# Kernel tuning notes

Hardware: AMD Instinct MI355X
Metric: run time of the kernel (lower is better)

The kernel has to match this reference:

```python
import jax, jax.numpy as jnp
from jax import lax
import numpy as np

B, CIN, H, S = 32, 16, 64, 128
TAU = 0.5


def _conv1d(x, w, b, dilation):
    # x: [B, C, S], w: [O, I, K] -> [B, O, S], stride 1, SAME padding (matches torch padding='same')
    y = lax.conv_general_dilated(x, w, window_strides=(1,), padding='SAME',
                                 rhs_dilation=(dilation,),
                                 dimension_numbers=('NCH', 'OIH', 'NCH'))
    return y + b[None, :, None]


def setup_inputs() -> dict:
    key = jax.random.key(0)
    ks = jax.random.split(key, 16)
    def w(k, shape, fan_in):
        return jax.random.normal(k, shape, jnp.float32) * (1.0 / np.sqrt(fan_in))
    inp = {
        'data': jax.random.normal(ks[0], (B, 1, CIN, S), jnp.float32),
        'conv11_w': w(ks[1], (H, CIN, 1), CIN), 'conv11_b': jnp.zeros((H,), jnp.float32),
        'conv12_w': w(ks[2], (H, H, 3), H * 3), 'conv12_b': jnp.zeros((H,), jnp.float32),
        'conv21_w': w(ks[3], (H, CIN, 1), CIN), 'conv21_b': jnp.zeros((H,), jnp.float32),
        'conv22_w': w(ks[4], (H, H, 5), H * 5), 'conv22_b': jnp.zeros((H,), jnp.float32),
        'conv31_w': w(ks[5], (H, CIN, 5), CIN * 5), 'conv31_b': jnp.zeros((H,), jnp.float32),
        'fc_final_w': w(ks[6], (H, 3 * H), 3 * H), 'fc_final_b': jnp.zeros((H,), jnp.float32),
        'fc1_w': w(ks[7], (H, 2 * H), 2 * H), 'fc1_b': jnp.zeros((H,), jnp.float32),
        'fc2_w': w(ks[8], (2, H), H), 'fc2_b': jnp.zeros((2,), jnp.float32),
        # pre-sampled uniform noise for gumbel-softmax (deterministic reference)
        'gumbel_u': jax.random.uniform(ks[9], (B, S * S, 2), jnp.float32, 1e-7, 1.0 - 1e-7),
    }
    return inp


def reference(data, conv11_w, conv11_b, conv12_w, conv12_b, conv21_w, conv21_b,
              conv22_w, conv22_b, conv31_w, conv31_b, fc_final_w, fc_final_b,
              fc1_w, fc1_b, fc2_w, fc2_b, gumbel_u):
    x = data[:, 0].astype(jnp.float32)                      # [B, CIN, S]
    x1 = _conv1d(_conv1d(x, conv11_w, conv11_b, 1), conv12_w, conv12_b, 3)
    x2 = _conv1d(_conv1d(x, conv21_w, conv21_b, 1), conv22_w, conv22_b, 5)
    x3 = _conv1d(x, conv31_w, conv31_b, 1)
    h = jnp.concatenate([x1, x2, x3], axis=1)               # [B, 3H, S]
    h = jnp.swapaxes(h, 1, 2)                               # [B, S, 3H]
    h = jax.nn.relu(h @ fc_final_w.T + fc_final_b)          # [B, S, H]

    # one-hot matmuls are exact gathers: rec rows = repeat, send cols = tile
    rows = jnp.repeat(jnp.arange(S), S)                     # [S*S]
    cols = jnp.tile(jnp.arange(S), S)                       # [S*S]
    receivers = h[:, rows]                                  # [B, S*S, H]
    senders = h[:, cols]                                    # [B, S*S, H]
    e = jnp.concatenate([senders, receivers], axis=2)       # [B, S*S, 2H]
    e = jax.nn.relu(e @ fc1_w.T + fc1_b)
    logits = e @ fc2_w.T + fc2_b                            # [B, S*S, 2]

    # gumbel-softmax, hard=True (straight-through)
    g = -jnp.log(-jnp.log(gumbel_u))
    y_soft = jax.nn.softmax((logits + g) / TAU, axis=-1)
    y_hard = jax.nn.one_hot(jnp.argmax(y_soft, axis=-1), 2, dtype=y_soft.dtype)
    y = lax.stop_gradient(y_hard - y_soft) + y_soft

    a = y[..., 0].reshape(-1, S, S)                         # [B, S, S]
    keep = jnp.triu(jnp.ones((S, S), bool), k=1)            # zero lower tri and diagonal
    return jnp.where(keep, a, jnp.zeros((), a.dtype))
```

## Files before the change

kernel.cpp:

```cpp
#include <hip/hip_runtime.h>
#include <math.h>

#define BB   32
#define CIN  16
#define HH   64
#define SS   128

typedef double f64x4 __attribute__((ext_vector_type(4)));
#define MFMA64(a,b,c) __builtin_amdgcn_mfma_f64_16x16x4f64((a),(b),(c),0,0,0)

__global__ __launch_bounds__(256) void prep_weights(
    const float* __restrict__ w11, const float* __restrict__ w21,
    const float* __restrict__ w12, const float* __restrict__ w22,
    const float* __restrict__ w31, const float* __restrict__ wf,
    const float* __restrict__ w1,  float* __restrict__ W)
{
    int i = blockIdx.x * 256 + threadIdx.x;
    if (i < 1024)       { int k=i>>4, c=i&15;                  W[c*64+k]          = w11[i]; }
    else if (i < 2048)  { int j=i-1024;  int k=j>>4, c=j&15;   W[1024 + c*64+k]   = w21[j]; }
    else if (i < 14336) { int j=i-2048;  int n=j/192, r=j-192*n; W[2048 + r*64+n] = w12[j]; }
    else if (i < 34816) { int j=i-14336; int n=j/320, r=j-320*n; W[14336 + r*64+n]= w22[j]; }
    else if (i < 43008) { int j=i-34816; int r=j>>6, n=j&63;   W[34816 + j] = (r<80)? w31[n*80+r] : 0.f; }
    else if (i < 55296) { int j=i-43008; int n=j/192, r=j-192*n; W[43008 + r*64+n]= wf[j]; }
    else if (i < 59392) { int j=i-55296; int n=j>>6, m=j&63;   W[55296 + m*64+n]  = w1[n*128+m]; }
    else if (i < 63488) { int j=i-59392; int n=j>>6, m=j&63;   W[59392 + m*64+n]  = w1[n*128+64+m]; }
}

__device__ __forceinline__ void issue_pf(float* pf, const float* __restrict__ Wsrc,
                                         int c, int t) {
    if (c < 15) {
        const float* s = Wsrc + 2048 + c * 4096 + t;
        #pragma unroll
        for (int q = 0; q < 16; ++q) pf[q] = s[q * 256];
    }
}
__device__ __forceinline__ void commit_pf(const float* pf, double* Wf, int t,
                                          int mB1, int mB2) {
    #pragma unroll
    for (int q = 0; q < 16; ++q) {
        int e = t + 256 * q, k = e >> 6, n = e & 63;
        Wf[((k>>2)<<8) + ((n>>4)<<6) + (k&3)*mB1 + (n&15)*mB2] = (double)pf[q];
    }
}
__device__ __forceinline__ void mfma_chunk(const double* pA, const double* pB,
                                           f64x4& a0, f64x4& a1, f64x4& a2, f64x4& a3) {
    #pragma unroll
    for (int s = 0; s < 16; s += 4) {
        a0 = MFMA64(pA[(s+0)*64], pB[(s+0)*256], a0);
        a1 = MFMA64(pA[(s+1)*64], pB[(s+1)*256], a1);
        a2 = MFMA64(pA[(s+2)*64], pB[(s+2)*256], a2);
        a3 = MFMA64(pA[(s+3)*64], pB[(s+3)*256], a3);
    }
}

#define RUN_PHASE(NCH, ABASE, ...) do {                                        \
    f64x4 ac0{0,0,0,0}, ac1{0,0,0,0}, ac2{0,0,0,0}, ac3{0,0,0,0};              \
    for (int ch_ = 0; ch_ < (NCH); ++ch_) {                                    \
        commit_pf(pf, Wf, t, mB1, mB2);                                        \
        __syncthreads();                                                       \
        ++cc; issue_pf(pf, Wsrc, cc, t);                                       \
        mfma_chunk((ABASE) + ch_*1024 + lane, Wf + wofs + lane,                \
                   ac0, ac1, ac2, ac3);                                        \
        __syncthreads();                                                       \
    }                                                                          \
    f64x4 acm = (ac0 + ac1) + (ac2 + ac3);                                     \
    __VA_ARGS__                                                                \
} while (0)

__global__ __launch_bounds__(256, 1) void fused_front(
    const float* __restrict__ x,
    const float* __restrict__ b11, const float* __restrict__ b12,
    const float* __restrict__ b21, const float* __restrict__ b22,
    const float* __restrict__ b31, const float* __restrict__ bf,
    const float* __restrict__ b1,  const float* __restrict__ Wsrc,
    double* __restrict__ Qg, double* __restrict__ Pg)
{
    const int b  = blockIdx.y;
    const int s0 = blockIdx.x * 16;
    const int t  = threadIdx.x;
    const int lane = t & 63, wave = t >> 6, wofs = wave << 6;

    __shared__ float  xl[CIN][37];
    __shared__ double t1e[48 * 64];
    __shared__ double t2e[80 * 64];
    __shared__ double x3e[32 * 64];
    __shared__ double Wf[4096];
    __shared__ double x123[16][196];
    double* he = x3e;

    int rowi[4], colj[4], mA1, mA2, mB1, mB2;
    {
        double lv = (double)lane;
        f64x4 zz{0.0, 0.0, 0.0, 0.0};
        f64x4 d1 = MFMA64(lv, 1.0, zz);
        f64x4 d2 = MFMA64(1.0, lv, zz);
        int am = ((((int)d1[0]) & 3) == 0);
        int bm = ((((int)d2[0]) & 3) == 0);
        for (int r = 0; r < 4; ++r) {
            int v1 = (int)d1[r], v2 = (int)d2[r];
            rowi[r] = (am ? (v1 - 96) >> 2 : (v1 - 6) >> 4) & 15;
            colj[r] = (bm ? (v2 - 96) >> 2 : (v2 - 6) >> 4) & 15;
        }
        mA1 = am ? 16 : 1;  mA2 = am ? 1 : 4;
        mB1 = bm ? 16 : 1;  mB2 = bm ? 1 : 4;
    }

    float pf[16];
    int cc = 0;
    issue_pf(pf, Wsrc, 0, t);

    float* wA = (float*)Wf;
    for (int e = t; e < 2048; e += 256) wA[e] = Wsrc[e];
    for (int e = t; e < CIN * 36; e += 256) {
        int c = e / 36, col = e - c * 36;
        int g = s0 - 10 + col;
        xl[c][col] = (g >= 0 && g < SS) ? x[(b * CIN + c) * SS + g] : 0.f;
    }
    __syncthreads();

    for (int e = t; e < 1408; e += 256) {
        int k = e & 63, col = e >> 6;
        int g = s0 - 3 + col;
        double val = 0.0;
        if (g >= 0 && g < SS) {
            double u0 = (double)b11[k], u1 = 0.0;
            #pragma unroll
            for (int c = 0; c < CIN; c += 2) {
                u0 += (double)xl[c][col + 7]     * (double)wA[c * 64 + k];
                u1 += (double)xl[c + 1][col + 7] * (double)wA[(c + 1) * 64 + k];
            }
            val = u0 + u1;
        }
        #pragma unroll
        for (int tp = 0; tp < 3; ++tp) {
            int p = col - 3 * tp;
            if (p >= 0 && p < 16) {
                int kk = k * 3 + tp;
                t1e[((kk>>2)<<6) + (kk&3)*mA1 + p*mA2] = val;
            }
        }
    }
    for (int e = t; e < 2304; e += 256) {
        int k = e & 63, col = e >> 6;
        int g = s0 - 10 + col;
        double val = 0.0;
        if (g >= 0 && g < SS) {
            double u0 = (double)b21[k], u1 = 0.0;
            #pragma unroll
            for (int c = 0; c < CIN; c += 2) {
                u0 += (double)xl[c][col]     * (double)wA[1024 + c * 64 + k];
                u1 += (double)xl[c + 1][col] * (double)wA[1024 + (c + 1) * 64 + k];
            }
            val = u0 + u1;
        }
        #pragma unroll
        for (int tp = 0; tp < 5; ++tp) {
            int p = col - 5 * tp;
            if (p >= 0 && p < 16) {
                int kk = k * 5 + tp;
                t2e[((kk>>2)<<6) + (kk&3)*mA1 + p*mA2] = val;
            }
        }
    }
    for (int e = t; e < 2048; e += 256) {
        int p = e & 15, kk = e >> 4;
        double val = 0.0;
        if (kk < 80) { int c = kk / 5, tp = kk - c * 5; val = (double)xl[c][p + 8 + tp]; }
        x3e[((kk>>2)<<6) + (kk&3)*mA1 + p*mA2] = val;
    }
    __syncthreads();

    RUN_PHASE(3, t1e, {
        for (int r = 0; r < 4; ++r) {
            int ch = (wave << 4) + colj[r];
            x123[rowi[r]][ch] = acm[r] + (double)b12[ch];
        }
    });
    RUN_PHASE(5, t2e, {
        for (int r = 0; r < 4; ++r) {
            int ch = (wave << 4) + colj[r];
            x123[rowi[r]][64 + ch] = acm[r] + (double)b22[ch];
        }
    });
    RUN_PHASE(2, x3e, {
        for (int r = 0; r < 4; ++r) {
            int ch = (wave << 4) + colj[r];
            x123[rowi[r]][128 + ch] = acm[r] + (double)b31[ch];
        }
    });
    __syncthreads();
    for (int e = t; e < 3072; e += 256) {
        int p = e & 15, k = e >> 4;
        t1e[((k>>2)<<6) + (k&3)*mA1 + p*mA2] = x123[p][k];
    }
    __syncthreads();
    RUN_PHASE(3, t1e, {
        for (int r = 0; r < 4; ++r) {
            int m = (wave << 4) + colj[r];
            double v = acm[r] + (double)bf[m];
            he[((m>>2)<<6) + (m&3)*mA1 + rowi[r]*mA2] = v > 0.0 ? v : 0.0;
        }
    });
    RUN_PHASE(1, he, {
        for (int r = 0; r < 4; ++r)
            Qg[((long)b * SS + s0 + rowi[r]) * HH + (wave << 4) + colj[r]] = acm[r];
    });
    RUN_PHASE(1, he, {
        for (int r = 0; r < 4; ++r) {
            int ch = (wave << 4) + colj[r];
            Pg[((long)b * SS + s0 + rowi[r]) * HH + ch] = acm[r] + (double)b1[ch];
        }
    });
}

__global__ __launch_bounds__(256) void edges(
    const double* __restrict__ Qg, const double* __restrict__ Pg,
    const float* __restrict__ w2, const float* __restrict__ b2,
    const float* __restrict__ gum, float* __restrict__ out)
{
    const int b   = blockIdx.y;
    const int tit = blockIdx.x >> 3;
    const int tjt = blockIdx.x & 7;
    const int t   = threadIdx.x;
    const int ti  = t >> 4, tj = t & 15;
    const int i   = tit * 16 + ti;
    const int j   = tjt * 16 + tj;
    float* op = out + ((long)b * SS + i) * SS + j;

    if (tjt < tit) { *op = 0.0f; return; }

    __shared__ double Pl[16][66];
    __shared__ double Ql[16][66];
    __shared__ double dwl[64];

    if (t < 64) dwl[t] = (double)w2[t] - (double)w2[64 + t];
    for (int idx = t; idx < 1024; idx += 256) {
        int r = idx >> 6, c = idx & 63;
        Pl[r][c] = Pg[((long)b * SS + tit * 16 + r) * HH + c];
        Ql[r][c] = Qg[((long)b * SS + tjt * 16 + r) * HH + c];
    }
    __syncthreads();

    if (j <= i) { *op = 0.0f; return; }

    long e = (long)b * SS * SS + (long)i * SS + j;
    double u0 = (double)gum[e * 2 + 0];
    double u1 = (double)gum[e * 2 + 1];
    double base = ((double)b2[0] - (double)b2[1]) - log(-log(u0)) + log(-log(u1));
    double a0 = 0.0, a1 = 0.0;
    #pragma unroll
    for (int k = 0; k < 64; k += 2) {
        double v0 = Pl[ti][k]     + Ql[tj][k];
        double v1 = Pl[ti][k + 1] + Ql[tj][k + 1];
        v0 = v0 > 0.0 ? v0 : 0.0;
        v1 = v1 > 0.0 ? v1 : 0.0;
        a0 += v0 * dwl[k];
        a1 += v1 * dwl[k + 1];
    }
    *op = (base + a0 + a1 >= 0.0) ? 1.0f : 0.0f;
}

extern "C" void kernel_launch(void* const* d_in, const int* in_sizes, int n_in,
                              void* d_out, int out_size, void* d_ws, size_t ws_size,
                              hipStream_t stream) {
    const float* data = (const float*)d_in[0];
    const float* w11  = (const float*)d_in[1];
    const float* b11  = (const float*)d_in[2];
    const float* w12  = (const float*)d_in[3];
    const float* b12  = (const float*)d_in[4];
    const float* w21  = (const float*)d_in[5];
    const float* b21  = (const float*)d_in[6];
    const float* w22  = (const float*)d_in[7];
    const float* b22  = (const float*)d_in[8];
    const float* w31  = (const float*)d_in[9];
    const float* b31  = (const float*)d_in[10];
    const float* wf   = (const float*)d_in[11];
    const float* bf   = (const float*)d_in[12];
    const float* w1   = (const float*)d_in[13];
    const float* b1   = (const float*)d_in[14];
    const float* w2   = (const float*)d_in[15];
    const float* b2   = (const float*)d_in[16];
    const float* gum  = (const float*)d_in[17];
    float* out = (float*)d_out;

    double* Qg = (double*)d_ws;
    double* Pg = Qg + (long)BB * SS * HH;
    float*  Wt = (float*)(Pg + (long)BB * SS * HH);

    prep_weights<<<248, 256, 0, stream>>>(w11, w21, w12, w22, w31, wf, w1, Wt);
    fused_front<<<dim3(8, BB), 256, 0, stream>>>(
        data, b11, b12, b21, b22, b31, bf, b1, Wt, Qg, Pg);
    edges<<<dim3(64, BB), 256, 0, stream>>>(Qg, Pg, w2, b2, gum, out);
}
```

Before: 51.66 us.

## Register-prefetch weight fragments in front kernel; compute edges in fp32 with fp64 fallback

In the front kernel, the per-chunk staging of weights through shared memory, with its two barriers per chunk, is removed. Each lane now loads its own B-fragment straight from global memory into double-buffered registers ahead of each MFMA chunk. In the edge kernel, the 64-wide relu-dot and the gumbel log terms are computed in fp32 with vectorized float2 loads. It falls back to the exact fp64 path only when the fp32 total is within a small threshold of zero. This trades extra per-lane global loads and a divergent fallback branch for fewer syncs and cheaper arithmetic, and the threshold has to be large enough to keep results matching.

New measurement: 51.39 us. About the same (-0.5%).

```diff
diff --git a/kernel.cpp b/kernel.cpp
--- a/kernel.cpp
+++ b/kernel.cpp
@@ -26,46 +26,21 @@
     else if (i < 63488) { int j=i-59392; int n=j>>6, m=j&63;   W[59392 + m*64+n]  = w1[n*128+64+m]; }
 }
 
-__device__ __forceinline__ void issue_pf(float* pf, const float* __restrict__ Wsrc,
-                                         int c, int t) {
-    if (c < 15) {
-        const float* s = Wsrc + 2048 + c * 4096 + t;
-        #pragma unroll
-        for (int q = 0; q < 16; ++q) pf[q] = s[q * 256];
-    }
-}
-__device__ __forceinline__ void commit_pf(const float* pf, double* Wf, int t,
-                                          int mB1, int mB2) {
+__device__ __forceinline__ void loadB(float* dst, const float* __restrict__ Bb, int c) {
+    const float* s = Bb + c * 4096;
     #pragma unroll
-    for (int q = 0; q < 16; ++q) {
-        int e = t + 256 * q, k = e >> 6, n = e & 63;
-        Wf[((k>>2)<<8) + ((n>>4)<<6) + (k&3)*mB1 + (n&15)*mB2] = (double)pf[q];
-    }
-}
-__device__ __forceinline__ void mfma_chunk(const double* pA, const double* pB,
+    for (int q = 0; q < 16; ++q) dst[q] = s[q * 256];
+}
+__device__ __forceinline__ void mfma_chunk(const double* pA, const float* cb,
                                            f64x4& a0, f64x4& a1, f64x4& a2, f64x4& a3) {
     #pragma unroll
     for (int s = 0; s < 16; s += 4) {
-        a0 = MFMA64(pA[(s+0)*64], pB[(s+0)*256], a0);
-        a1 = MFMA64(pA[(s+1)*64], pB[(s+1)*256], a1);
-        a2 = MFMA64(pA[(s+2)*64], pB[(s+2)*256], a2);
-        a3 = MFMA64(pA[(s+3)*64], pB[(s+3)*256], a3);
-    }
-}
-
-#define RUN_PHASE(NCH, ABASE, ...) do {                                        \
-    f64x4 ac0{0,0,0,0}, ac1{0,0,0,0}, ac2{0,0,0,0}, ac3{0,0,0,0};              \
-    for (int ch_ = 0; ch_ < (NCH); ++ch_) {                                    \
-        commit_pf(pf, Wf, t, mB1, mB2);                                        \
-        __syncthreads();                                                       \
-        ++cc; issue_pf(pf, Wsrc, cc, t);                                       \
-        mfma_chunk((ABASE) + ch_*1024 + lane, Wf + wofs + lane,                \
-                   ac0, ac1, ac2, ac3);                                        \
-        __syncthreads();                                                       \
-    }                                                                          \
-    f64x4 acm = (ac0 + ac1) + (ac2 + ac3);                                     \
-    __VA_ARGS__                                                                \
-} while (0)
+        a0 = MFMA64(pA[(s+0)*64], (double)cb[s+0], a0);
+        a1 = MFMA64(pA[(s+1)*64], (double)cb[s+1], a1);
+        a2 = MFMA64(pA[(s+2)*64], (double)cb[s+2], a2);
+        a3 = MFMA64(pA[(s+3)*64], (double)cb[s+3], a3);
+    }
+}
 
 __global__ __launch_bounds__(256, 1) void fused_front(
     const float* __restrict__ x,
@@ -78,17 +53,17 @@
     const int b  = blockIdx.y;
     const int s0 = blockIdx.x * 16;
     const int t  = threadIdx.x;
-    const int lane = t & 63, wave = t >> 6, wofs = wave << 6;
+    const int lane = t & 63, wave = t >> 6;
 
     __shared__ float  xl[CIN][37];
+    __shared__ float  wA[2048];
     __shared__ double t1e[48 * 64];
     __shared__ double t2e[80 * 64];
     __shared__ double x3e[32 * 64];
-    __shared__ double Wf[4096];
     __shared__ double x123[16][196];
     double* he = x3e;
 
-    int rowi[4], colj[4], mA1, mA2, mB1, mB2;
+    int rowi[4], colj[4], mA1, mA2, bn, bkk;
     {
         double lv = (double)lane;
         f64x4 zz{0.0, 0.0, 0.0, 0.0};
@@ -102,14 +77,14 @@
             colj[r] = (bm ? (v2 - 96) >> 2 : (v2 - 6) >> 4) & 15;
         }
         mA1 = am ? 16 : 1;  mA2 = am ? 1 : 4;
-        mB1 = bm ? 16 : 1;  mB2 = bm ? 1 : 4;
-    }
-
-    float pf[16];
-    int cc = 0;
-    issue_pf(pf, Wsrc, 0, t);
-
-    float* wA = (float*)Wf;
+        bn  = bm ? (lane & 15) : (lane >> 2);
+        bkk = bm ? (lane >> 4) : (lane & 3);
+    }
+    const float* Bb = Wsrc + 2048 + bkk * 64 + (wave << 4) + bn;
+
+    float bufa[16], bufb[16];
+    loadB(bufa, Bb, 0);
+
     for (int e = t; e < 2048; e += 256) wA[e] = Wsrc[e];
     for (int e = t; e < CIN * 36; e += 256) {
         int c = e / 36, col = e - c * 36;
@@ -170,47 +145,75 @@
     }
     __syncthreads();
 
-    RUN_PHASE(3, t1e, {
+    {
+        f64x4 a0{0,0,0,0}, a1{0,0,0,0}, a2{0,0,0,0}, a3{0,0,0,0};
+        loadB(bufb, Bb, 1);  mfma_chunk(t1e + lane,        bufa, a0,a1,a2,a3);
+        loadB(bufa, Bb, 2);  mfma_chunk(t1e + 1024 + lane, bufb, a0,a1,a2,a3);
+        loadB(bufb, Bb, 3);  mfma_chunk(t1e + 2048 + lane, bufa, a0,a1,a2,a3);
+        f64x4 acm = (a0 + a1) + (a2 + a3);
         for (int r = 0; r < 4; ++r) {
             int ch = (wave << 4) + colj[r];
             x123[rowi[r]][ch] = acm[r] + (double)b12[ch];
         }
-    });
-    RUN_PHASE(5, t2e, {
+    }
+    {
+        f64x4 a0{0,0,0,0}, a1{0,0,0,0}, a2{0,0,0,0}, a3{0,0,0,0};
+        loadB(bufa, Bb, 4);  mfma_chunk(t2e + lane,        bufb, a0,a1,a2,a3);
+        loadB(bufb, Bb, 5);  mfma_chunk(t2e + 1024 + lane, bufa, a0,a1,a2,a3);
+        loadB(bufa, Bb, 6);  mfma_chunk(t2e + 2048 + lane, bufb, a0,a1,a2,a3);
+        loadB(bufb, Bb, 7);  mfma_chunk(t2e + 3072 + lane, bufa, a0,a1,a2,a3);
+        loadB(bufa, Bb, 8);  mfma_chunk(t2e + 4096 + lane, bufb, a0,a1,a2,a3);
+        f64x4 acm = (a0 + a1) + (a2 + a3);
         for (int r = 0; r < 4; ++r) {
             int ch = (wave << 4) + colj[r];
             x123[rowi[r]][64 + ch] = acm[r] + (double)b22[ch];
         }
-    });
-    RUN_PHASE(2, x3e, {
+    }
+    {
+        f64x4 a0{0,0,0,0}, a1{0,0,0,0}, a2{0,0,0,0}, a3{0,0,0,0};
+        loadB(bufb, Bb, 9);  mfma_chunk(x3e + lane,        bufa, a0,a1,a2,a3);
+        loadB(bufa, Bb, 10); mfma_chunk(x3e + 1024 + lane, bufb, a0,a1,a2,a3);
+        f64x4 acm = (a0 + a1) + (a2 + a3);
         for (int r = 0; r < 4; ++r) {
             int ch = (wave << 4) + colj[r];
             x123[rowi[r]][128 + ch] = acm[r] + (double)b31[ch];
         }
-    });
+    }
     __syncthreads();
     for (int e = t; e < 3072; e += 256) {
         int p = e & 15, k = e >> 4;
         t1e[((k>>2)<<6) + (k&3)*mA1 + p*mA2] = x123[p][k];
     }
     __syncthreads();
-    RUN_PHASE(3, t1e, {
+    {
+        f64x4 a0{0,0,0,0}, a1{0,0,0,0}, a2{0,0,0,0}, a3{0,0,0,0};
+        loadB(bufb, Bb, 11); mfma_chunk(t1e + lane,        bufa, a0,a1,a2,a3);
+        loadB(bufa, Bb, 12); mfma_chunk(t1e + 1024 + lane, bufb, a0,a1,a2,a3);
+        loadB(bufb, Bb, 13); mfma_chunk(t1e + 2048 + lane, bufa, a0,a1,a2,a3);
+        f64x4 acm = (a0 + a1) + (a2 + a3);
         for (int r = 0; r < 4; ++r) {
             int m = (wave << 4) + colj[r];
             double v = acm[r] + (double)bf[m];
             he[((m>>2)<<6) + (m&3)*mA1 + rowi[r]*mA2] = v > 0.0 ? v : 0.0;
         }
-    });
-    RUN_PHASE(1, he, {
+    }
+    __syncthreads();
+    {
+        f64x4 a0{0,0,0,0}, a1{0,0,0,0}, a2{0,0,0,0}, a3{0,0,0,0};
+        loadB(bufa, Bb, 14); mfma_chunk(he + lane, bufb, a0,a1,a2,a3);
+        f64x4 acm = (a0 + a1) + (a2 + a3);
         for (int r = 0; r < 4; ++r)
             Qg[((long)b * SS + s0 + rowi[r]) * HH + (wave << 4) + colj[r]] = acm[r];
-    });
-    RUN_PHASE(1, he, {
+    }
+    {
+        f64x4 a0{0,0,0,0}, a1{0,0,0,0}, a2{0,0,0,0}, a3{0,0,0,0};
+        mfma_chunk(he + lane, bufa, a0,a1,a2,a3);
+        f64x4 acm = (a0 + a1) + (a2 + a3);
         for (int r = 0; r < 4; ++r) {
             int ch = (wave << 4) + colj[r];
             Pg[((long)b * SS + s0 + rowi[r]) * HH + ch] = acm[r] + (double)b1[ch];
         }
-    });
+    }
 }
 
 __global__ __launch_bounds__(256) void edges(
@@ -229,35 +232,50 @@
 
     if (tjt < tit) { *op = 0.0f; return; }
 
-    __shared__ double Pl[16][66];
-    __shared__ double Ql[16][66];
-    __shared__ double dwl[64];
-
-    if (t < 64) dwl[t] = (double)w2[t] - (double)w2[64 + t];
+    __shared__ float Plf[16][68];
+    __shared__ float Qlf[16][68];
+    __shared__ float dwl[64];
+
+    if (t < 64) dwl[t] = w2[t] - w2[64 + t];
     for (int idx = t; idx < 1024; idx += 256) {
         int r = idx >> 6, c = idx & 63;
-        Pl[r][c] = Pg[((long)b * SS + tit * 16 + r) * HH + c];
-        Ql[r][c] = Qg[((long)b * SS + tjt * 16 + r) * HH + c];
+        Plf[r][c] = (float)Pg[((long)b * SS + tit * 16 + r) * HH + c];
+        Qlf[r][c] = (float)Qg[((long)b * SS + tjt * 16 + r) * HH + c];
     }
     __syncthreads();
 
     if (j <= i) { *op = 0.0f; return; }
 
     long e = (long)b * SS * SS + (long)i * SS + j;
-    double u0 = (double)gum[e * 2 + 0];
-    double u1 = (double)gum[e * 2 + 1];
-    double base = ((double)b2[0] - (double)b2[1]) - log(-log(u0)) + log(-log(u1));
-    double a0 = 0.0, a1 = 0.0;
+    const float2 uv = *(const float2*)(gum + e * 2);
+    float basef = (b2[0] - b2[1]) - logf(-logf(uv.x)) + logf(-logf(uv.y));
+
+    const float2* Pr = (const float2*)(&Plf[ti][0]);
+    const float2* Qr = (const float2*)(&Qlf[tj][0]);
+    const float2* Dr = (const float2*)dwl;
+    float s0 = 0.f, s1 = 0.f;
     #pragma unroll
-    for (int k = 0; k < 64; k += 2) {
-        double v0 = Pl[ti][k]     + Ql[tj][k];
-        double v1 = Pl[ti][k + 1] + Ql[tj][k + 1];
-        v0 = v0 > 0.0 ? v0 : 0.0;
-        v1 = v1 > 0.0 ? v1 : 0.0;
-        a0 += v0 * dwl[k];
-        a1 += v1 * dwl[k + 1];
-    }
-    *op = (base + a0 + a1 >= 0.0) ? 1.0f : 0.0f;
+    for (int k2 = 0; k2 < 32; ++k2) {
+        float2 pv = Pr[k2], qv = Qr[k2], dv = Dr[k2];
+        float v0 = pv.x + qv.x; v0 = v0 > 0.f ? v0 : 0.f;
+        float v1 = pv.y + qv.y; v1 = v1 > 0.f ? v1 : 0.f;
+        s0 += v0 * dv.x; s1 += v1 * dv.y;
+    }
+    float tot = basef + s0 + s1;
+
+    if (fabsf(tot) < 3e-3f) {
+        const double* Prd = Pg + ((long)b * SS + i) * HH;
+        const double* Qrd = Qg + ((long)b * SS + j) * HH;
+        double acc = (double)b2[0] - (double)b2[1]
+                   - log(-log((double)uv.x)) + log(-log((double)uv.y));
+        for (int k = 0; k < 64; ++k) {
+            double v = Prd[k] + Qrd[k];
+            if (v > 0.0) acc += v * ((double)w2[k] - (double)w2[64 + k]);
+        }
+        *op = (acc >= 0.0) ? 1.0f : 0.0f;
+    } else {
+        *op = (tot >= 0.f) ? 1.0f : 0.0f;
+    }
 }
 
 extern "C" void kernel_launch(void* const* d_in, const int* in_sizes, int n_in,
```
